# Performance work log

Measured on AMD Instinct MI355X. Metric: run time of the kernel, lower is better.

## Reference

```python
import jax, jax.numpy as jnp
import numpy as np

N_NODES = 100000
N_EDGES = 3200000
D_IN = 128
D_OUT = 128


def setup_inputs() -> dict:
    key = jax.random.key(0)
    kx, kw, kb, kr, kc, kv = jax.random.split(key, 6)
    x = jax.random.normal(kx, (N_NODES, D_IN), dtype=jnp.float32)
    W = jax.random.normal(kw, (D_OUT, D_IN), dtype=jnp.float32) * (1.0 / np.sqrt(D_IN))
    b = jax.random.normal(kb, (D_OUT,), dtype=jnp.float32) * 0.01
    adj_rows = jax.random.randint(kr, (N_EDGES,), 0, N_NODES, dtype=jnp.int32)
    adj_cols = jax.random.randint(kc, (N_EDGES,), 0, N_NODES, dtype=jnp.int32)
    adj_vals = jax.random.uniform(kv, (N_EDGES,), dtype=jnp.float32)
    return {"x": x, "W": W, "b": b, "adj_rows": adj_rows,
            "adj_cols": adj_cols, "adj_vals": adj_vals}


def reference(x, W, b, adj_rows, adj_cols, adj_vals):
    # linear: out = x @ W.T + b   -> [N, D_OUT]
    out = jnp.einsum('ni,oi->no', x, W) + b
    # spmm(adj, out): row r = sum over edges (r, c, v) of v * out[c]
    gathered = out[adj_cols] * adj_vals[:, None]          # [E, D_OUT]
    agg = jax.ops.segment_sum(gathered, adj_rows, num_segments=x.shape[0])
    return jax.nn.elu(agg)
```

## Files before the change

### kernel.cpp

```cpp
#include <hip/hip_runtime.h>
#include <hip/hip_bf16.h>
#include <cmath>

#define RPB      32
#define FB_CAP   1280
#define SB_SHIFT 11
#define NSB_MAX  64
#define TILE     2048
#define CH_PER_SB 34

typedef __attribute__((ext_vector_type(8))) short short8;
typedef __attribute__((ext_vector_type(4))) float floatx4;

__device__ __forceinline__ unsigned short f2bf(float f) {
    unsigned int u = __float_as_uint(f);
    u += 0x7FFFu + ((u >> 16) & 1u);
    return (unsigned short)(u >> 16);
}

__global__ __launch_bounds__(256) void gemm_mfma_kernel(
    const float* __restrict__ x, const float* __restrict__ W,
    const float* __restrict__ b, unsigned short* __restrict__ Yb, int N)
{
    __shared__ unsigned short Wb[128][136];
    __shared__ unsigned short Xb[64][136];
    const int t    = threadIdx.x;
    const int wave = t >> 6;
    const int lane = t & 63;
    const int col  = lane & 15;
    const int quad = lane >> 4;
    const int rowbase = blockIdx.x * 64;

#pragma unroll
    for (int i = 0; i < 16; ++i) {
        const int idx = t + 256 * i;
        const int o = idx >> 5, k4 = (idx & 31) * 4;
        const float4 v = *(const float4*)&W[(size_t)idx * 4];
        Wb[o][k4 + 0] = f2bf(v.x); Wb[o][k4 + 1] = f2bf(v.y);
        Wb[o][k4 + 2] = f2bf(v.z); Wb[o][k4 + 3] = f2bf(v.w);
    }
#pragma unroll
    for (int i = 0; i < 8; ++i) {
        const int idx = t + 256 * i;
        const int row = idx >> 5, k4 = (idx & 31) * 4;
        const int gr = rowbase + row;
        float4 v = make_float4(0.f, 0.f, 0.f, 0.f);
        if (gr < N) v = *(const float4*)&x[(size_t)gr * 128 + k4];
        Xb[row][k4 + 0] = f2bf(v.x); Xb[row][k4 + 1] = f2bf(v.y);
        Xb[row][k4 + 2] = f2bf(v.z); Xb[row][k4 + 3] = f2bf(v.w);
    }
    __syncthreads();

    float bias[8];
#pragma unroll
    for (int nt = 0; nt < 8; ++nt) bias[nt] = b[nt * 16 + col];

    floatx4 acc[8] = {};
    const int mrow = wave * 16;
#pragma unroll
    for (int k0 = 0; k0 < 128; k0 += 32) {
        const short8 a = *(const short8*)&Xb[mrow + col][k0 + quad * 8];
#pragma unroll
        for (int nt = 0; nt < 8; ++nt) {
            const short8 bf = *(const short8*)&Wb[nt * 16 + col][k0 + quad * 8];
            acc[nt] = __builtin_amdgcn_mfma_f32_16x16x32_bf16(a, bf, acc[nt], 0, 0, 0);
        }
    }
#pragma unroll
    for (int nt = 0; nt < 8; ++nt) {
#pragma unroll
        for (int reg = 0; reg < 4; ++reg) {
            const int gr = rowbase + mrow + quad * 4 + reg;
            if (gr < N)
                Yb[(size_t)gr * 128 + nt * 16 + col] = f2bf(acc[nt][reg] + bias[nt]);
        }
    }
}

__global__ __launch_bounds__(256) void init_cursor_kernel(
    int* __restrict__ cursor1, int* __restrict__ cursor2, int SB_CAP, int NB)
{
    const int i = blockIdx.x * blockDim.x + threadIdx.x;
    if (i < NSB_MAX) cursor1[i] = i * SB_CAP;
    if (i < NB)      cursor2[i] = i * FB_CAP;
}

__global__ __launch_bounds__(256) void pass1_kernel(
    const int* __restrict__ rows, const int* __restrict__ cols,
    const float* __restrict__ vals, int* __restrict__ cursor1,
    int2* __restrict__ pairs1, int E)
{
    __shared__ int2 sbuf[TILE];
    __shared__ unsigned char sbin[TILE];
    __shared__ unsigned short perm[TILE];
    __shared__ int hist[NSB_MAX], off[NSB_MAX], gbase[NSB_MAX], cur[NSB_MAX];
    const int t  = threadIdx.x;
    const int lo = blockIdx.x * TILE;
    const int cnt = min(TILE, E - lo);

    if (t < NSB_MAX) hist[t] = 0;
    __syncthreads();
    for (int i = t; i < cnt; i += 256) {
        const int   r = rows[lo + i];
        const int   c = cols[lo + i];
        const float v = vals[lo + i];
        sbuf[i] = make_int2(((r & 2047) << 17) | c, __float_as_int(v));
        const int bb = r >> SB_SHIFT;
        sbin[i] = (unsigned char)bb;
        atomicAdd(&hist[bb], 1);
    }
    __syncthreads();
    if (t == 0) {
        int run = 0;
        for (int k = 0; k < NSB_MAX; ++k) { off[k] = run; cur[k] = run; run += hist[k]; }
    }
    __syncthreads();
    if (t < NSB_MAX && hist[t] > 0) gbase[t] = atomicAdd(&cursor1[t], hist[t]);
    __syncthreads();
    for (int i = t; i < cnt; i += 256) {
        const int pos = atomicAdd(&cur[sbin[i]], 1);
        perm[pos] = (unsigned short)i;
    }
    __syncthreads();
    for (int i = t; i < cnt; i += 256) {
        const int src = perm[i];
        const int bb  = sbin[src];
        pairs1[gbase[bb] + (i - off[bb])] = sbuf[src];
    }
}

__global__ __launch_bounds__(256) void pass2_kernel(
    const int* __restrict__ cursor1, int* __restrict__ cursor2,
    const int2* __restrict__ pairs1, int2* __restrict__ pairs2, int SB_CAP)
{
    __shared__ int2 sbuf[TILE];
    __shared__ unsigned short perm[TILE];
    __shared__ int hist[64], off[64], gbase[64], cur[64];
    const int t   = threadIdx.x;
    const int sb  = blockIdx.x / CH_PER_SB;
    const int ch  = blockIdx.x % CH_PER_SB;
    const int base = sb * SB_CAP;
    const int scnt = cursor1[sb] - base;
    const int csz  = (scnt + CH_PER_SB - 1) / CH_PER_SB;
    const int lo   = ch * csz;
    const int cnt  = max(0, min(csz, scnt - lo));

    if (t < 64) hist[t] = 0;
    __syncthreads();
    for (int i = t; i < cnt; i += 256) {
        const int2 p = pairs1[base + lo + i];
        sbuf[i] = p;
        atomicAdd(&hist[(unsigned)p.x >> 22], 1);
    }
    __syncthreads();
    if (t == 0) {
        int run = 0;
        for (int k = 0; k < 64; ++k) { off[k] = run; cur[k] = run; run += hist[k]; }
    }
    __syncthreads();
    if (t < 64 && hist[t] > 0)
        gbase[t] = atomicAdd(&cursor2[sb * 64 + t], hist[t]);
    __syncthreads();
    for (int i = t; i < cnt; i += 256) {
        const int pos = atomicAdd(&cur[(unsigned)sbuf[i].x >> 22], 1);
        perm[pos] = (unsigned short)i;
    }
    __syncthreads();
    for (int i = t; i < cnt; i += 256) {
        const int2 p = sbuf[perm[i]];
        const int bb = (unsigned)p.x >> 22;
        pairs2[gbase[bb] + (i - off[bb])] = make_int2(p.x & 0x3FFFFF, p.y);
    }
}

__global__ __launch_bounds__(256) void sortgather_kernel(
    const int* __restrict__ cursor2, const int2* __restrict__ pairs2,
    const unsigned int* __restrict__ Yu, float* __restrict__ out, int N)
{
    __shared__ __align__(16) int2 sbuf[FB_CAP];
    __shared__ __align__(16) int2 dbuf[FB_CAP + 4];
    __shared__ int hist[RPB];
    __shared__ int off[RPB];
    __shared__ int cur[RPB];
    __shared__ int rowtick;
    const int b    = blockIdx.x;
    const int t    = threadIdx.x;
    const int lane = t & 63;
    const int slot = b * FB_CAP;
    int cnt = cursor2[b] - slot;
    if (cnt > FB_CAP) cnt = FB_CAP;

    if (t < RPB) hist[t] = 0;
    if (t == 0) rowtick = 0;
    __syncthreads();
    for (int i = t; i < cnt; i += 256) {
        const int2 p = pairs2[slot + i];
        sbuf[i] = p;
        atomicAdd(&hist[p.x >> 17], 1);
    }
    __syncthreads();
    if (t == 0) {
        int run = 0;
#pragma unroll
        for (int k = 0; k < RPB; ++k) { off[k] = run; cur[k] = run; run += hist[k]; }
    }
    __syncthreads();
    for (int i = t; i < cnt; i += 256) {
        const int2 p   = sbuf[i];
        const int  pos = atomicAdd(&cur[p.x >> 17], 1);
        dbuf[pos] = make_int2(p.x & 0x1FFFF, p.y);
    }
    if (t < 4) dbuf[cnt + t] = make_int2(0, 0);
    __syncthreads();

    const int sub   = lane >> 4;
    const int qlane = lane & 15;

    for (;;) {
        int rl = 0;
        if (lane == 0) rl = atomicAdd(&rowtick, 1);
        rl = __shfl(rl, 0);
        if (rl >= RPB) break;
        const int gr = b * RPB + rl;
        if (gr >= N) continue;
        const int s = off[rl];
        const int e = s + hist[rl];

        float acc0 = 0.f, acc1 = 0.f, acc2 = 0.f, acc3 = 0.f;
        float acc4 = 0.f, acc5 = 0.f, acc6 = 0.f, acc7 = 0.f;
#pragma unroll 2
        for (int j = s; j < e; j += 4) {
            const int2 p = dbuf[j + sub];
            float v = __int_as_float(p.y);
            v = (j + sub < e) ? v : 0.0f;
            const uint4 y = *(const uint4*)&Yu[((unsigned)p.x << 6) + qlane * 4];
            acc0 = fmaf(v, __uint_as_float(y.x << 16), acc0);
            acc1 = fmaf(v, __uint_as_float(y.x & 0xFFFF0000u), acc1);
            acc2 = fmaf(v, __uint_as_float(y.y << 16), acc2);
            acc3 = fmaf(v, __uint_as_float(y.y & 0xFFFF0000u), acc3);
            acc4 = fmaf(v, __uint_as_float(y.z << 16), acc4);
            acc5 = fmaf(v, __uint_as_float(y.z & 0xFFFF0000u), acc5);
            acc6 = fmaf(v, __uint_as_float(y.w << 16), acc6);
            acc7 = fmaf(v, __uint_as_float(y.w & 0xFFFF0000u), acc7);
        }
        acc0 += __shfl_xor(acc0, 32); acc1 += __shfl_xor(acc1, 32);
        acc2 += __shfl_xor(acc2, 32); acc3 += __shfl_xor(acc3, 32);
        acc4 += __shfl_xor(acc4, 32); acc5 += __shfl_xor(acc5, 32);
        acc6 += __shfl_xor(acc6, 32); acc7 += __shfl_xor(acc7, 32);
        acc0 += __shfl_xor(acc0, 16); acc1 += __shfl_xor(acc1, 16);
        acc2 += __shfl_xor(acc2, 16); acc3 += __shfl_xor(acc3, 16);
        acc4 += __shfl_xor(acc4, 16); acc5 += __shfl_xor(acc5, 16);
        acc6 += __shfl_xor(acc6, 16); acc7 += __shfl_xor(acc7, 16);

        if (lane < 16) {
            float4 o0, o1;
            o0.x = acc0 > 0.f ? acc0 : __expf(acc0) - 1.f;
            o0.y = acc1 > 0.f ? acc1 : __expf(acc1) - 1.f;
            o0.z = acc2 > 0.f ? acc2 : __expf(acc2) - 1.f;
            o0.w = acc3 > 0.f ? acc3 : __expf(acc3) - 1.f;
            o1.x = acc4 > 0.f ? acc4 : __expf(acc4) - 1.f;
            o1.y = acc5 > 0.f ? acc5 : __expf(acc5) - 1.f;
            o1.z = acc6 > 0.f ? acc6 : __expf(acc6) - 1.f;
            o1.w = acc7 > 0.f ? acc7 : __expf(acc7) - 1.f;
            float* po = &out[(size_t)gr * 128 + qlane * 8];
            *(float4*)po       = o0;
            *(float4*)(po + 4) = o1;
        }
    }
}

__global__ __launch_bounds__(256) void gemm_bias_kernel(
    const float* __restrict__ x, const float* __restrict__ W,
    const float* __restrict__ b, float* __restrict__ Y, int N)
{
    __shared__ float Wt[128][130];
    const int tid  = threadIdx.x;
    const int wave = tid >> 6;
    const int lane = tid & 63;
    for (int i = tid; i < 128 * 128; i += 256) {
        const int o = i >> 7, k = i & 127;
        Wt[k][o] = W[i];
    }
    __syncthreads();
    const float2 bv = *(const float2*)&b[2 * lane];
    for (int row = blockIdx.x * 4 + wave; row < N; row += gridDim.x * 4) {
        float acc0 = 0.f, acc1 = 0.f;
        for (int k = 0; k < 128; ++k) {
            const float2 w = *(const float2*)&Wt[k][2 * lane];
            const float xv = x[(size_t)row * 128 + k];
            acc0 = fmaf(xv, w.x, acc0);
            acc1 = fmaf(xv, w.y, acc1);
        }
        float2 o2; o2.x = acc0 + bv.x; o2.y = acc1 + bv.y;
        *(float2*)&Y[(size_t)row * 128 + 2 * lane] = o2;
    }
}

__global__ __launch_bounds__(256) void scatter_kernel(
    const int* __restrict__ rows, const int* __restrict__ cols,
    const float* __restrict__ vals, const float* __restrict__ Y,
    float* __restrict__ out, int E)
{
    const long long gid = (long long)blockIdx.x * blockDim.x + threadIdx.x;
    const int wid  = (int)(gid >> 6);
    const int lane = threadIdx.x & 63;
    if (wid >= E) return;
    const int   r = rows[wid];
    const int   c = cols[wid];
    const float v = vals[wid];
    const float2 y = *(const float2*)&Y[(size_t)c * 128 + 2 * lane];
    float* po = &out[(size_t)r * 128 + 2 * lane];
    atomicAdd(po,     v * y.x);
    atomicAdd(po + 1, v * y.y);
}

__global__ __launch_bounds__(256) void elu_kernel(float* __restrict__ out, int n4)
{
    int i = blockIdx.x * blockDim.x + threadIdx.x;
    const int stride = gridDim.x * blockDim.x;
    float4* p = (float4*)out;
    for (; i < n4; i += stride) {
        float4 v = p[i];
        v.x = v.x > 0.f ? v.x : expf(v.x) - 1.f;
        v.y = v.y > 0.f ? v.y : expf(v.y) - 1.f;
        v.z = v.z > 0.f ? v.z : expf(v.z) - 1.f;
        v.w = v.w > 0.f ? v.w : expf(v.w) - 1.f;
        p[i] = v;
    }
}

extern "C" void kernel_launch(void* const* d_in, const int* in_sizes, int n_in,
                              void* d_out, int out_size, void* d_ws, size_t ws_size,
                              hipStream_t stream)
{
    const float* x    = (const float*)d_in[0];
    const float* W    = (const float*)d_in[1];
    const float* b    = (const float*)d_in[2];
    const int*   rows = (const int*)d_in[3];
    const int*   cols = (const int*)d_in[4];
    const float* vals = (const float*)d_in[5];
    float* out = (float*)d_out;

    const int N   = in_sizes[0] / 128;
    const int E   = in_sizes[3];
    const int NB  = (N + RPB - 1) / RPB;
    const int NSB = (N + (1 << SB_SHIFT) - 1) >> SB_SHIFT;

    const int sb_mean = (E + NSB - 1) / NSB;
    int sbsig = 1; while (sbsig * sbsig < sb_mean) ++sbsig;
    const int SB_CAP = (sb_mean + 10 * sbsig + 63) & ~63;

    auto align256 = [](size_t v) { return (v + 255) & ~(size_t)255; };
    const size_t offPairs2 = 0;
    const size_t szPairs2  = (size_t)NB * FB_CAP * 8;
    const size_t offShared = align256(offPairs2 + szPairs2);
    const size_t szShared  = (size_t)NSB * SB_CAP * 8 > (size_t)N * 256
                           ? (size_t)NSB * SB_CAP * 8 : (size_t)N * 256;
    const size_t offCur1   = align256(offShared + szShared);
    const size_t offCur2   = align256(offCur1 + NSB_MAX * 4);
    const size_t need      = offCur2 + (size_t)NB * 4;

    const bool csr_ok = (need <= ws_size) && (NSB <= NSB_MAX) &&
                        ((long long)E <= (long long)NB * 1056) &&
                        (SB_CAP <= CH_PER_SB * TILE);

    if (csr_ok) {
        int2* pairs2        = (int2*)((char*)d_ws + offPairs2);
        int2* pairs1        = (int2*)((char*)d_ws + offShared);
        unsigned short* Yb  = (unsigned short*)((char*)d_ws + offShared);
        int*  cursor1       = (int*)((char*)d_ws + offCur1);
        int*  cursor2       = (int*)((char*)d_ws + offCur2);

        init_cursor_kernel<<<(NB + 255) / 256, 256, 0, stream>>>(cursor1, cursor2,
                                                                 SB_CAP, NB);
        pass1_kernel<<<(E + TILE - 1) / TILE, 256, 0, stream>>>(rows, cols, vals,
                                                                cursor1, pairs1, E);
        pass2_kernel<<<NSB * CH_PER_SB, 256, 0, stream>>>(cursor1, cursor2,
                                                          pairs1, pairs2, SB_CAP);
        gemm_mfma_kernel<<<(N + 63) / 64, 256, 0, stream>>>(x, W, b, Yb, N);
        sortgather_kernel<<<NB, 256, 0, stream>>>(cursor2, pairs2,
                                                  (const unsigned int*)Yb, out, N);
    } else {
        float* Y = (float*)d_ws;
        hipMemsetAsync(d_out, 0, (size_t)out_size * sizeof(float), stream);
        gemm_bias_kernel<<<512, 256, 0, stream>>>(x, W, b, Y, N);
        scatter_kernel<<<(E + 3) / 4, 256, 0, stream>>>(rows, cols, vals, Y, out, E);
        elu_kernel<<<1024, 256, 0, stream>>>(out, out_size / 4);
    }
}
```

Before: 317.2 us.

## Precast W to bf16 once, stage GEMM output in LDS, simplify bucket scatter

Converts W to bf16 a single time inside the init kernel, so each GEMM block loads pre-converted weights with 16-byte copies instead of converting 64KB of fp32. GEMM results are written to LDS first and then stored to global memory as coalesced 16-byte rows, replacing scattered 2-byte stores. The two bucketing passes drop the prefix-sum, permutation array and extra barriers and instead scatter each element directly using per-bucket LDS atomic cursors. This gives up locality of the scatter writes and the order of elements within a bucket.

New measurement: 314.1 us. No clear change (-1.0%).

```diff
diff --git a/kernel.cpp b/kernel.cpp
--- a/kernel.cpp
+++ b/kernel.cpp
@@ -19,11 +19,11 @@
 }
 
 __global__ __launch_bounds__(256) void gemm_mfma_kernel(
-    const float* __restrict__ x, const float* __restrict__ W,
+    const float* __restrict__ x, const unsigned short* __restrict__ Wbg,
     const float* __restrict__ b, unsigned short* __restrict__ Yb, int N)
 {
-    __shared__ unsigned short Wb[128][136];
-    __shared__ unsigned short Xb[64][136];
+    __shared__ __align__(16) unsigned short Wb[128][136];
+    __shared__ __align__(16) unsigned short Xb[64][136];
     const int t    = threadIdx.x;
     const int wave = t >> 6;
     const int lane = t & 63;
@@ -32,12 +32,10 @@
     const int rowbase = blockIdx.x * 64;
 
 #pragma unroll
-    for (int i = 0; i < 16; ++i) {
+    for (int i = 0; i < 8; ++i) {
         const int idx = t + 256 * i;
-        const int o = idx >> 5, k4 = (idx & 31) * 4;
-        const float4 v = *(const float4*)&W[(size_t)idx * 4];
-        Wb[o][k4 + 0] = f2bf(v.x); Wb[o][k4 + 1] = f2bf(v.y);
-        Wb[o][k4 + 2] = f2bf(v.z); Wb[o][k4 + 3] = f2bf(v.w);
+        const int o = idx >> 4, k8 = (idx & 15) * 8;
+        *(uint4*)&Wb[o][k8] = *(const uint4*)&Wbg[idx * 8];
     }
 #pragma unroll
     for (int i = 0; i < 8; ++i) {
@@ -69,20 +67,35 @@
 #pragma unroll
     for (int nt = 0; nt < 8; ++nt) {
 #pragma unroll
-        for (int reg = 0; reg < 4; ++reg) {
-            const int gr = rowbase + mrow + quad * 4 + reg;
-            if (gr < N)
-                Yb[(size_t)gr * 128 + nt * 16 + col] = f2bf(acc[nt][reg] + bias[nt]);
-        }
+        for (int reg = 0; reg < 4; ++reg)
+            Xb[mrow + quad * 4 + reg][nt * 16 + col] = f2bf(acc[nt][reg] + bias[nt]);
+    }
+    __syncthreads();
+#pragma unroll
+    for (int i = 0; i < 4; ++i) {
+        const int idx = t + 256 * i;
+        const int row = idx >> 4, c16 = (idx & 15) * 8;
+        const int gr  = rowbase + row;
+        if (gr < N)
+            *(uint4*)&Yb[(size_t)gr * 128 + c16] = *(const uint4*)&Xb[row][c16];
     }
 }
 
 __global__ __launch_bounds__(256) void init_cursor_kernel(
-    int* __restrict__ cursor1, int* __restrict__ cursor2, int SB_CAP, int NB)
+    int* __restrict__ cursor1, int* __restrict__ cursor2, int SB_CAP, int NB,
+    const float* __restrict__ W, unsigned short* __restrict__ Wbg)
 {
     const int i = blockIdx.x * blockDim.x + threadIdx.x;
     if (i < NSB_MAX) cursor1[i] = i * SB_CAP;
     if (i < NB)      cursor2[i] = i * FB_CAP;
+    const int stride = gridDim.x * blockDim.x;
+    for (int j = i; j < 128 * 128 / 4; j += stride) {
+        const float4 v = ((const float4*)W)[j];
+        uint2 u;
+        u.x = (unsigned)f2bf(v.x) | ((unsigned)f2bf(v.y) << 16);
+        u.y = (unsigned)f2bf(v.z) | ((unsigned)f2bf(v.w) << 16);
+        ((uint2*)Wbg)[j] = u;
+    }
 }
 
 __global__ __launch_bounds__(256) void pass1_kernel(
@@ -92,8 +105,7 @@
 {
     __shared__ int2 sbuf[TILE];
     __shared__ unsigned char sbin[TILE];
-    __shared__ unsigned short perm[TILE];
-    __shared__ int hist[NSB_MAX], off[NSB_MAX], gbase[NSB_MAX], cur[NSB_MAX];
+    __shared__ int hist[NSB_MAX], cur[NSB_MAX];
     const int t  = threadIdx.x;
     const int lo = blockIdx.x * TILE;
     const int cnt = min(TILE, E - lo);
@@ -110,22 +122,11 @@
         atomicAdd(&hist[bb], 1);
     }
     __syncthreads();
-    if (t == 0) {
-        int run = 0;
-        for (int k = 0; k < NSB_MAX; ++k) { off[k] = run; cur[k] = run; run += hist[k]; }
-    }
-    __syncthreads();
-    if (t < NSB_MAX && hist[t] > 0) gbase[t] = atomicAdd(&cursor1[t], hist[t]);
+    if (t < NSB_MAX) cur[t] = atomicAdd(&cursor1[t], hist[t]);
     __syncthreads();
     for (int i = t; i < cnt; i += 256) {
         const int pos = atomicAdd(&cur[sbin[i]], 1);
-        perm[pos] = (unsigned short)i;
-    }
-    __syncthreads();
-    for (int i = t; i < cnt; i += 256) {
-        const int src = perm[i];
-        const int bb  = sbin[src];
-        pairs1[gbase[bb] + (i - off[bb])] = sbuf[src];
+        pairs1[pos] = sbuf[i];
     }
 }
 
@@ -134,8 +135,7 @@
     const int2* __restrict__ pairs1, int2* __restrict__ pairs2, int SB_CAP)
 {
     __shared__ int2 sbuf[TILE];
-    __shared__ unsigned short perm[TILE];
-    __shared__ int hist[64], off[64], gbase[64], cur[64];
+    __shared__ int hist[64], cur[64];
     const int t   = threadIdx.x;
     const int sb  = blockIdx.x / CH_PER_SB;
     const int ch  = blockIdx.x % CH_PER_SB;
@@ -153,23 +153,13 @@
         atomicAdd(&hist[(unsigned)p.x >> 22], 1);
     }
     __syncthreads();
-    if (t == 0) {
-        int run = 0;
-        for (int k = 0; k < 64; ++k) { off[k] = run; cur[k] = run; run += hist[k]; }
-    }
-    __syncthreads();
-    if (t < 64 && hist[t] > 0)
-        gbase[t] = atomicAdd(&cursor2[sb * 64 + t], hist[t]);
-    __syncthreads();
-    for (int i = t; i < cnt; i += 256) {
-        const int pos = atomicAdd(&cur[(unsigned)sbuf[i].x >> 22], 1);
-        perm[pos] = (unsigned short)i;
-    }
-    __syncthreads();
-    for (int i = t; i < cnt; i += 256) {
-        const int2 p = sbuf[perm[i]];
+    if (t < 64) cur[t] = atomicAdd(&cursor2[sb * 64 + t], hist[t]);
+    __syncthreads();
+    for (int i = t; i < cnt; i += 256) {
+        const int2 p = sbuf[i];
         const int bb = (unsigned)p.x >> 22;
-        pairs2[gbase[bb] + (i - off[bb])] = make_int2(p.x & 0x3FFFFF, p.y);
+        const int pos = atomicAdd(&cur[bb], 1);
+        pairs2[pos] = make_int2(p.x & 0x3FFFFF, p.y);
     }
 }
 
@@ -358,7 +348,8 @@
                            ? (size_t)NSB * SB_CAP * 8 : (size_t)N * 256;
     const size_t offCur1   = align256(offShared + szShared);
     const size_t offCur2   = align256(offCur1 + NSB_MAX * 4);
-    const size_t need      = offCur2 + (size_t)NB * 4;
+    const size_t offWb     = align256(offCur2 + (size_t)NB * 4);
+    const size_t need      = offWb + 128 * 128 * 2;
 
     const bool csr_ok = (need <= ws_size) && (NSB <= NSB_MAX) &&
                         ((long long)E <= (long long)NB * 1056) &&
@@ -370,14 +361,15 @@
         unsigned short* Yb  = (unsigned short*)((char*)d_ws + offShared);
         int*  cursor1       = (int*)((char*)d_ws + offCur1);
         int*  cursor2       = (int*)((char*)d_ws + offCur2);
+        unsigned short* Wbg = (unsigned short*)((char*)d_ws + offWb);
 
         init_cursor_kernel<<<(NB + 255) / 256, 256, 0, stream>>>(cursor1, cursor2,
-                                                                 SB_CAP, NB);
+                                                                 SB_CAP, NB, W, Wbg);
         pass1_kernel<<<(E + TILE - 1) / TILE, 256, 0, stream>>>(rows, cols, vals,
                                                                 cursor1, pairs1, E);
         pass2_kernel<<<NSB * CH_PER_SB, 256, 0, stream>>>(cursor1, cursor2,
                                                           pairs1, pairs2, SB_CAP);
-        gemm_mfma_kernel<<<(N + 63) / 64, 256, 0, stream>>>(x, W, b, Yb, N);
+        gemm_mfma_kernel<<<(N + 63) / 64, 256, 0, stream>>>(x, Wbg, b, Yb, N);
         sortgather_kernel<<<NB, 256, 0, stream>>>(cursor2, pairs2,
                                                   (const unsigned int*)Yb, out, N);
     } else {
```
